# Performance work log

Hardware: AMD Instinct MI355X
Metric: run time of the kernel (lower is better)

## Reference

```python
import jax, jax.numpy as jnp
import numpy as np

N_AE = 64
N_GRAPHS = 4096
N_ELE = 16384
EPS = 1e-5


def _seg_mean(v, idx, num_segments):
    s = jax.ops.segment_sum(v, idx, num_segments=num_segments)
    c = jax.ops.segment_sum(jnp.ones((v.shape[0], 1), v.dtype), idx, num_segments=num_segments)
    return s / jnp.maximum(c, 1.0)


def _batchnorm(h, gamma, beta):
    mu = jnp.mean(h, axis=0)
    var = jnp.mean(jnp.square(h - mu), axis=0)  # biased, as torch BN training fwd
    return (h - mu) * jax.lax.rsqrt(var + EPS) * gamma + beta


def _dist_layer(x, dist_feat, atom_idx, ele_idx, W, b, gamma, beta):
    # x: [N, 2*n_ae]
    pa = jax.nn.relu(_seg_mean(x[:, :N_AE], atom_idx, N_GRAPHS))[atom_idx]   # [N, n_ae]
    pe = jax.nn.relu(_seg_mean(x[:, N_AE:], ele_idx, N_ELE))[ele_idx]        # [N, n_ae]
    h = jnp.concatenate([dist_feat, pa, pe], axis=1)                          # [N, n_de+2*n_ae]
    h = h @ W.T + b                                                           # [N, 2*n_ae]
    h = _batchnorm(h, gamma, beta)
    return jax.nn.relu(h + x)


def setup_inputs() -> dict:
    key = jax.random.key(0)
    ks = jax.random.split(key, 12)
    N = 500000
    n_re = 64
    n_be = 64
    d = 2 * N_AE
    inp = {
        "x": jax.random.normal(ks[0], (N, d), jnp.float32),
        "rdf_feat": jax.random.normal(ks[1], (N, n_re), jnp.float32),
        "bdf_feat": jax.random.normal(ks[2], (N, n_be), jnp.float32),
        "atom_idx": jnp.sort(jax.random.randint(ks[3], (N,), 0, N_GRAPHS)),
        "ele_idx": jax.random.randint(ks[4], (N,), 0, N_ELE),
        "rdf_W": jax.random.normal(ks[5], (d, n_re + d), jnp.float32) * 0.05,
        "rdf_b": jnp.zeros((d,), jnp.float32),
        "rdf_gamma": jnp.ones((d,), jnp.float32),
        "rdf_beta": jnp.zeros((d,), jnp.float32),
        "bdf_W": jax.random.normal(ks[6], (d, n_be + d), jnp.float32) * 0.05,
        "bdf_b": jnp.zeros((d,), jnp.float32),
        "bdf_gamma": jnp.ones((d,), jnp.float32),
        "bdf_beta": jnp.zeros((d,), jnp.float32),
        "fc_W": jax.random.normal(ks[7], (d, 2 * d), jnp.float32) * 0.05,
        "fc_b": jnp.zeros((d,), jnp.float32),
    }
    return inp


def reference(x, rdf_feat, bdf_feat, atom_idx, ele_idx,
              rdf_W, rdf_b, rdf_gamma, rdf_beta,
              bdf_W, bdf_b, bdf_gamma, bdf_beta,
              fc_W, fc_b):
    x1 = _dist_layer(x, rdf_feat, atom_idx, ele_idx, rdf_W, rdf_b, rdf_gamma, rdf_beta)
    x2 = _dist_layer(x, bdf_feat, atom_idx, ele_idx, bdf_W, bdf_b, bdf_gamma, bdf_beta)
    h = jnp.concatenate([x1, x2], axis=1)  # [N, 4*n_ae]
    return jax.nn.relu(h @ fc_W.T + fc_b)  # [N, 2*n_ae]
```

## Files before the change

### kernel.cpp

```cpp
#include <hip/hip_runtime.h>
#include <hip/hip_bf16.h>

#define N_GRAPHS 4096
#define N_ELE 16384
#define EPS 1e-5f

#define A_TAB_OFF 0
#define A_CNT_OFF 262144
#define E_TAB_OFF 266240
#define E_CNT_OFF 1314816
#define STAT_OFF  1331200
#define ZERO_WORDS 1347584
#define A_TABH_OFF 1347584
#define E_TABH_OFF 1478656
#define W1PK_OFF  2002944
#define FCPK_OFF  2027520
#define SCALE_OFF 2043904
#define SHIFT_OFF 2044160
#define WS_WORDS  2044416

typedef __attribute__((ext_vector_type(8))) short bf16x8;
typedef __attribute__((ext_vector_type(4))) float f32x4;

__device__ __forceinline__ float bf2f(unsigned s) { return __uint_as_float(s << 16); }
__device__ __forceinline__ unsigned f2bf(float f) {
  unsigned u = __float_as_uint(f);
  return (u + 0x7fffu + ((u >> 16) & 1u)) >> 16;
}

__global__ void k_prep(const float* __restrict__ W1, const float* __restrict__ W2,
                       const float* __restrict__ fcW, float* __restrict__ ws) {
  int tid = blockIdx.x * 512 + threadIdx.x;
  if (tid < 49152) {
    unsigned short* wpk = (unsigned short*)(ws + W1PK_OFF);
    int L = tid / 24576, rem = tid % 24576;
    int ct = rem / 3072, rem2 = rem % 3072;
    int i = rem2 >> 9, lane = (rem2 >> 3) & 63, j = rem2 & 7;
    int zkb = L ? (i + 2) : (i < 2 ? i : i + 2);
    int zk = zkb * 32 + ((lane >> 4) << 3) + j;
    int kp = L ? (zk - 64) : (zk < 64 ? zk : zk - 64);
    int col = ct * 16 + (lane & 15);
    const float* W = L ? W2 : W1;
    wpk[tid] = (unsigned short)f2bf(W[col * 192 + kp]);
  } else {
    int idx = tid - 49152;
    unsigned short* fpk = (unsigned short*)(ws + FCPK_OFF);
    int ct = idx >> 12, kb = (idx >> 9) & 7, lane = (idx >> 3) & 63, j = idx & 7;
    fpk[idx] = (unsigned short)f2bf(fcW[(ct * 16 + (lane & 15)) * 256 + kb * 32 + ((lane >> 4) << 3) + j]);
  }
}

__global__ void k_seg(const float* __restrict__ x, const int* __restrict__ aidx,
                      const int* __restrict__ eidx, float* __restrict__ ws, int N) {
  float* A_tab = ws + A_TAB_OFF; float* A_cnt = ws + A_CNT_OFF;
  float* E_tab = ws + E_TAB_OFF; float* E_cnt = ws + E_CNT_OFF;
  int t = threadIdx.x;
  int c = t & 63, p = (t >> 6) & 1, s = t >> 7;
  int r0 = blockIdx.x * 256;
  int rend = min(r0 + 256, N);
  if (p == 0) {
    float acc = 0.f, cnt = 0.f; int cur = -1;
    for (int r = r0 + s; r < rend; r += 2) {
      int a = aidx[r];
      float v = x[(size_t)r * 128 + c];
      if (a != cur) {
        if (cur >= 0) { atomicAdd(&A_tab[cur * 64 + c], acc); if (c == 0) atomicAdd(&A_cnt[cur], cnt); }
        cur = a; acc = v; cnt = 1.f;
      } else { acc += v; cnt += 1.f; }
    }
    if (cur >= 0) { atomicAdd(&A_tab[cur * 64 + c], acc); if (c == 0) atomicAdd(&A_cnt[cur], cnt); }
  } else {
    for (int r = r0 + s; r < rend; r += 2) {
      int e = eidx[r];
      float v = x[(size_t)r * 128 + 64 + c];
      atomicAdd(&E_tab[e * 64 + c], v);
      if (c == 0) atomicAdd(&E_cnt[e], 1.f);
    }
  }
}

__global__ void k_fin(float* __restrict__ ws) {
  int i = blockIdx.x * 256 + threadIdx.x;
  unsigned* w32 = (unsigned*)ws;
  if (i < 131072) {
    int e = 2 * i;
    float cnt = fmaxf(ws[A_CNT_OFF + (e >> 6)], 1.f);
    float v0 = fmaxf(ws[A_TAB_OFF + e] / cnt, 0.f);
    float v1 = fmaxf(ws[A_TAB_OFF + e + 1] / cnt, 0.f);
    w32[A_TABH_OFF + i] = f2bf(v0) | (f2bf(v1) << 16);
  }
  if (i < 524288) {
    int e = 2 * i;
    float cnt = fmaxf(ws[E_CNT_OFF + (e >> 6)], 1.f);
    float v0 = fmaxf(ws[E_TAB_OFF + e] / cnt, 0.f);
    float v1 = fmaxf(ws[E_TAB_OFF + e + 1] / cnt, 0.f);
    w32[E_TABH_OFF + i] = f2bf(v0) | (f2bf(v1) << 16);
  }
}

__global__ __launch_bounds__(512) void k_gemm(
    const float* __restrict__ rdf, const float* __restrict__ bdf,
    const int* __restrict__ aidx, const int* __restrict__ eidx,
    float* __restrict__ ws, unsigned* __restrict__ outp, int N) {
  __shared__ __align__(16) char smem[33792];
  const unsigned short* Atabh = (const unsigned short*)(ws + A_TABH_OFF);
  const unsigned short* Etabh = (const unsigned short*)(ws + E_TABH_OFF);
  int t = threadIdx.x;
  int row0 = blockIdx.x * 64;
  {
    int r = t >> 3, g = t & 7;
    int row = row0 + r;
    unsigned wv[16];
    if (row < N) {
      if (g < 4) {
        const float* src = ((g < 2) ? rdf : bdf) + (size_t)row * 64 + (g & 1) * 32;
        #pragma unroll
        for (int i = 0; i < 8; ++i) {
          float4 f = ((const float4*)src)[i];
          wv[i * 2]     = f2bf(f.x) | (f2bf(f.y) << 16);
          wv[i * 2 + 1] = f2bf(f.z) | (f2bf(f.w) << 16);
        }
      } else {
        const unsigned short* tab = (g < 6) ? Atabh : Etabh;
        int idx = (g < 6) ? aidx[row] : eidx[row];
        const uint4* srcv = (const uint4*)(tab + (size_t)idx * 64 + (g & 1) * 32);
        #pragma unroll
        for (int i = 0; i < 4; ++i) ((uint4*)wv)[i] = srcv[i];
      }
    } else {
      #pragma unroll
      for (int i = 0; i < 16; ++i) wv[i] = 0u;
    }
    int zc0 = g * 32;
    #pragma unroll
    for (int i = 0; i < 4; ++i) {
      int byte = r * 512 + (((zc0 + i * 8) * 2) ^ ((r & 7) << 4));
      *(uint4*)(smem + byte) = ((uint4*)wv)[i];
    }
  }
  __syncthreads();
  int l = t & 63, w = t >> 6;
  int L = w >> 2, ctp = w & 3;
  f32x4 acc[4][2];
  #pragma unroll
  for (int mt = 0; mt < 4; ++mt)
    #pragma unroll
    for (int cti = 0; cti < 2; ++cti) acc[mt][cti] = (f32x4){0.f, 0.f, 0.f, 0.f};
  const unsigned short* Wpk = (const unsigned short*)(ws + W1PK_OFF) + L * 24576;
  #pragma unroll
  for (int i = 0; i < 6; ++i) {
    int zkb = L ? (i + 2) : (i < 2 ? i : i + 2);
    bf16x8 af[4];
    #pragma unroll
    for (int mt = 0; mt < 4; ++mt) {
      int rr = mt * 16 + (l & 15);
      int byte = rr * 512 + ((zkb * 64 + ((l >> 4) << 4)) ^ ((rr & 7) << 4));
      af[mt] = *(const bf16x8*)(smem + byte);
    }
    #pragma unroll
    for (int cti = 0; cti < 2; ++cti) {
      int ct = ctp * 2 + cti;
      bf16x8 bfr = *(const bf16x8*)(Wpk + ((ct * 6 + i) * 64 + l) * 8);
      #pragma unroll
      for (int mt = 0; mt < 4; ++mt)
        acc[mt][cti] = __builtin_amdgcn_mfma_f32_16x16x32_bf16(af[mt], bfr, acc[mt][cti], 0, 0, 0);
    }
  }
  float ssum[2], ssq[2];
  #pragma unroll
  for (int cti = 0; cti < 2; ++cti) {
    float s = 0.f, q = 0.f;
    #pragma unroll
    for (int mt = 0; mt < 4; ++mt)
      #pragma unroll
      for (int rr = 0; rr < 4; ++rr) { float v = acc[mt][cti][rr]; s += v; q += v * v; }
    s += __shfl_xor(s, 16); s += __shfl_xor(s, 32);
    q += __shfl_xor(q, 16); q += __shfl_xor(q, 32);
    ssum[cti] = s; ssq[cti] = q;
  }
  {
    float* stat = ws + STAT_OFF + (blockIdx.x & 31) * 512;
    if (l < 16) {
      #pragma unroll
      for (int cti = 0; cti < 2; ++cti) {
        int gc = L * 128 + ctp * 32 + cti * 16 + l;
        atomicAdd(&stat[gc], ssum[cti]);
        atomicAdd(&stat[256 + gc], ssq[cti]);
      }
    }
  }
  __syncthreads();
  unsigned* hl = (unsigned*)smem;
  #pragma unroll
  for (int mt = 0; mt < 4; ++mt)
    #pragma unroll
    for (int cti = 0; cti < 2; ++cti)
      #pragma unroll
      for (int rr = 0; rr < 4; ++rr) {
        unsigned ub = f2bf(acc[mt][cti][rr]);
        unsigned pb = (unsigned)__shfl_xor((int)ub, 1);
        if (!(l & 1)) {
          int orow = mt * 16 + ((l >> 4) << 2) + rr;
          int colp = (L * 128 + ctp * 32 + cti * 16 + (l & 15)) >> 1;
          hl[orow * 132 + colp] = ub | (pb << 16);
        }
      }
  __syncthreads();
  #pragma unroll
  for (int p = 0; p < 4; ++p) {
    int e = p * 512 + t;
    int rr = e >> 5, v4 = e & 31;
    if (row0 + rr < N)
      ((uint4*)outp)[(size_t)(row0 + rr) * 32 + v4] = *(uint4*)&hl[rr * 132 + v4 * 4];
  }
}

__global__ void k_bnfin(const float* __restrict__ g1, const float* __restrict__ b1,
                        const float* __restrict__ g2, const float* __restrict__ b2,
                        float* __restrict__ ws, int N) {
  int c = threadIdx.x;
  float s = 0.f, q = 0.f;
  for (int m = 0; m < 32; ++m) { s += ws[STAT_OFF + m * 512 + c]; q += ws[STAT_OFF + m * 512 + 256 + c]; }
  float inv = 1.f / (float)N;
  float mu = s * inv;
  float var = fmaxf(q * inv - mu * mu, 0.f);
  int lyr = c >> 7, cc = c & 127;
  float ga = lyr ? g2[cc] : g1[cc];
  float be = lyr ? b2[cc] : b1[cc];
  float sc = ga * rsqrtf(var + EPS);
  ws[SCALE_OFF + c] = sc;
  ws[SHIFT_OFF + c] = be - mu * sc;
}

__global__ __launch_bounds__(512) void k_fc(
    const float* __restrict__ x, const float* __restrict__ fcb,
    float* __restrict__ ws, float* __restrict__ out, int N) {
  __shared__ __align__(16) char smem[33792];
  __shared__ float scsh[512];
  int t = threadIdx.x;
  int row0 = blockIdx.x * 64;
  scsh[t] = ws[SCALE_OFF + t];
  const unsigned* hp = (const unsigned*)out;
  int r = t >> 3, g = t & 7;
  int row = row0 + r;
  unsigned hw[16]; float xr[32];
  if (row < N) {
    #pragma unroll
    for (int i = 0; i < 4; ++i) ((uint4*)hw)[i] = ((const uint4*)(hp + (size_t)row * 128 + g * 16))[i];
    #pragma unroll
    for (int i = 0; i < 8; ++i) ((float4*)xr)[i] = ((const float4*)(x + (size_t)row * 128 + (g & 3) * 32))[i];
  } else {
    #pragma unroll
    for (int i = 0; i < 16; ++i) hw[i] = 0u;
    #pragma unroll
    for (int i = 0; i < 32; ++i) xr[i] = 0.f;
  }
  __syncthreads();
  {
    unsigned outw[16];
    if (row < N) {
      #pragma unroll
      for (int j = 0; j < 16; ++j) {
        int c = g * 32 + 2 * j;
        float lo = bf2f(hw[j] & 0xffffu) * scsh[c] + scsh[256 + c] + xr[2 * j];
        float hi = bf2f(hw[j] >> 16) * scsh[c + 1] + scsh[256 + c + 1] + xr[2 * j + 1];
        outw[j] = f2bf(fmaxf(lo, 0.f)) | (f2bf(fmaxf(hi, 0.f)) << 16);
      }
    } else {
      #pragma unroll
      for (int j = 0; j < 16; ++j) outw[j] = 0u;
    }
    #pragma unroll
    for (int i = 0; i < 4; ++i) {
      int byte = r * 512 + (((g * 32 + i * 8) * 2) ^ ((r & 7) << 4));
      *(uint4*)(smem + byte) = ((uint4*)outw)[i];
    }
  }
  __syncthreads();
  int l = t & 63, w = t >> 6;
  f32x4 acc[4];
  #pragma unroll
  for (int mt = 0; mt < 4; ++mt) acc[mt] = (f32x4){0.f, 0.f, 0.f, 0.f};
  const unsigned short* Fpk = (const unsigned short*)(ws + FCPK_OFF);
  #pragma unroll
  for (int kb = 0; kb < 8; ++kb) {
    bf16x8 bfr = *(const bf16x8*)(Fpk + ((w * 8 + kb) * 64 + l) * 8);
    #pragma unroll
    for (int mt = 0; mt < 4; ++mt) {
      int rr = mt * 16 + (l & 15);
      int byte = rr * 512 + ((kb * 64 + ((l >> 4) << 4)) ^ ((rr & 7) << 4));
      bf16x8 af = *(const bf16x8*)(smem + byte);
      acc[mt] = __builtin_amdgcn_mfma_f32_16x16x32_bf16(af, bfr, acc[mt], 0, 0, 0);
    }
  }
  float bias = fcb[(w << 4) + (l & 15)];
  __syncthreads();
  float* ol = (float*)smem;
  #pragma unroll
  for (int mt = 0; mt < 4; ++mt)
    #pragma unroll
    for (int rr = 0; rr < 4; ++rr)
      ol[(mt * 16 + ((l >> 4) << 2) + rr) * 132 + (w << 4) + (l & 15)] = fmaxf(acc[mt][rr] + bias, 0.f);
  __syncthreads();
  #pragma unroll
  for (int p = 0; p < 4; ++p) {
    int e = p * 512 + t;
    int rr = e >> 5, v4 = e & 31;
    if (row0 + rr < N)
      ((float4*)out)[(size_t)(row0 + rr) * 32 + v4] = *(float4*)&ol[rr * 132 + v4 * 4];
  }
}

extern "C" void kernel_launch(void* const* d_in, const int* in_sizes, int n_in,
                              void* d_out, int out_size, void* d_ws, size_t ws_size,
                              hipStream_t stream) {
  const float* x    = (const float*)d_in[0];
  const float* rdf  = (const float*)d_in[1];
  const float* bdf  = (const float*)d_in[2];
  const int*   aidx = (const int*)d_in[3];
  const int*   eidx = (const int*)d_in[4];
  const float* rdfW = (const float*)d_in[5];
  const float* rdfG = (const float*)d_in[7];
  const float* rdfBe= (const float*)d_in[8];
  const float* bdfW = (const float*)d_in[9];
  const float* bdfG = (const float*)d_in[11];
  const float* bdfBe= (const float*)d_in[12];
  const float* fcW  = (const float*)d_in[13];
  const float* fcB  = (const float*)d_in[14];
  float* out = (float*)d_out;
  float* ws  = (float*)d_ws;
  int N = in_sizes[0] / 128;

  hipMemsetAsync(d_ws, 0, (size_t)ZERO_WORDS * 4, stream);
  k_prep<<<160, 512, 0, stream>>>(rdfW, bdfW, fcW, ws);
  k_seg<<<(N + 255) / 256, 256, 0, stream>>>(x, aidx, eidx, ws, N);
  k_fin<<<2048, 256, 0, stream>>>(ws);
  int tiles = (N + 63) / 64;
  k_gemm<<<tiles, 512, 0, stream>>>(rdf, bdf, aidx, eidx, ws, (unsigned*)d_out, N);
  k_bnfin<<<1, 256, 0, stream>>>(rdfG, rdfBe, bdfG, bdfBe, ws, N);
  k_fc<<<tiles, 512, 0, stream>>>(x, fcB, ws, out, N);
}
```

Baseline: 472.2 us.

## Make GEMM and FC kernels persistent with double-buffered register prefetch

Both k_gemm and k_fc now launch a fixed grid of 512 persistent blocks that loop over 64-row tiles. While MFMA work runs on the current tile, the next tile's global loads, and the indices two tiles ahead, are prefetched into registers, then converted into a second 32KB LDS buffer. The LDS swizzle changes to an XOR slot scheme without padding, and bf16 conversion moves to the HIP intrinsic. The aim is to hide global load latency behind compute and avoid per-block launch cost. The cost is 64KB of LDS and more register pressure, which may limit occupancy; launch_bounds now asks for 4 waves.

```diff
diff --git a/kernel.cpp b/kernel.cpp
--- a/kernel.cpp
+++ b/kernel.cpp
@@ -27,6 +27,12 @@
   unsigned u = __float_as_uint(f);
   return (u + 0x7fffu + ((u >> 16) & 1u)) >> 16;
 }
+__device__ __forceinline__ unsigned pkbf(float a, float b) {
+  union { __hip_bfloat16 h; unsigned short u; } ca, cb;
+  ca.h = __float2bfloat16(a); cb.h = __float2bfloat16(b);
+  return (unsigned)ca.u | ((unsigned)cb.u << 16);
+}
+
 
 __global__ void k_prep(const float* __restrict__ W1, const float* __restrict__ W2,
                        const float* __restrict__ fcW, float* __restrict__ ws) {
@@ -98,120 +104,158 @@
   }
 }
 
-__global__ __launch_bounds__(512) void k_gemm(
+__device__ __forceinline__ void load_tile(const float* __restrict__ rdf, const float* __restrict__ bdf,
+    const unsigned short* __restrict__ Atabh, const unsigned short* __restrict__ Etabh,
+    int row, bool ok, int g, int idx, float4* fv) {
+  if (g < 4) {
+    if (ok) {
+      const float4* src = (const float4*)(((g < 2) ? rdf : bdf) + (size_t)row * 64 + (g & 1) * 32);
+      #pragma unroll
+      for (int i = 0; i < 8; ++i) fv[i] = src[i];
+    } else {
+      #pragma unroll
+      for (int i = 0; i < 8; ++i) fv[i] = (float4){0.f, 0.f, 0.f, 0.f};
+    }
+  } else {
+    if (ok) {
+      const float4* src = (const float4*)(((g < 6) ? Atabh : Etabh) + (size_t)idx * 64 + (g & 1) * 32);
+      #pragma unroll
+      for (int i = 0; i < 4; ++i) fv[i] = src[i];
+    } else {
+      #pragma unroll
+      for (int i = 0; i < 4; ++i) fv[i] = (float4){0.f, 0.f, 0.f, 0.f};
+    }
+  }
+}
+
+__device__ __forceinline__ void cvt_write(char* buf, int r, int g, const float4* fv) {
+  unsigned wv[16];
+  if (g < 4) {
+    #pragma unroll
+    for (int i = 0; i < 8; ++i) {
+      wv[2 * i]     = pkbf(fv[i].x, fv[i].y);
+      wv[2 * i + 1] = pkbf(fv[i].z, fv[i].w);
+    }
+  } else {
+    #pragma unroll
+    for (int i = 0; i < 4; ++i) ((float4*)wv)[i] = fv[i];
+  }
+  #pragma unroll
+  for (int i = 0; i < 4; ++i) {
+    int slot = ((g ^ r ^ i) & 7) | (i << 3);
+    *(uint4*)(buf + r * 512 + slot * 16) = ((uint4*)wv)[i];
+  }
+}
+
+__global__ __launch_bounds__(512, 4) void k_gemm(
     const float* __restrict__ rdf, const float* __restrict__ bdf,
     const int* __restrict__ aidx, const int* __restrict__ eidx,
-    float* __restrict__ ws, unsigned* __restrict__ outp, int N) {
-  __shared__ __align__(16) char smem[33792];
+    float* __restrict__ ws, unsigned* __restrict__ outp, int N, int nT) {
+  __shared__ __align__(16) char smem[65536];
   const unsigned short* Atabh = (const unsigned short*)(ws + A_TABH_OFF);
   const unsigned short* Etabh = (const unsigned short*)(ws + E_TABH_OFF);
   int t = threadIdx.x;
-  int row0 = blockIdx.x * 64;
+  int l = t & 63, w = t >> 6;
+  int r = t >> 3, g = t & 7;
+  int L = w >> 2, ctp = w & 3;
+  const unsigned short* WpkL = (const unsigned short*)(ws + W1PK_OFF) + L * 24576;
+  float* stat = ws + STAT_OFF + (blockIdx.x & 31) * 512;
+  int step = gridDim.x;
+  int tile = blockIdx.x;
+  float4 fv[8];
   {
-    int r = t >> 3, g = t & 7;
-    int row = row0 + r;
-    unsigned wv[16];
-    if (row < N) {
-      if (g < 4) {
-        const float* src = ((g < 2) ? rdf : bdf) + (size_t)row * 64 + (g & 1) * 32;
+    int row = tile * 64 + r; bool ok = row < N;
+    int idx0 = 0;
+    if (g >= 4 && ok) idx0 = ((g < 6) ? aidx : eidx)[row];
+    load_tile(rdf, bdf, Atabh, Etabh, row, ok, g, idx0, fv);
+  }
+  int idxN = 0;
+  {
+    int t2 = tile + step; int row2 = t2 * 64 + r;
+    if (g >= 4 && t2 < nT && row2 < N) idxN = ((g < 6) ? aidx : eidx)[row2];
+  }
+  cvt_write(smem, r, g, fv);
+  __syncthreads();
+  int cur = 0;
+  while (true) {
+    int nxt = tile + step;
+    bool hasN = nxt < nT;
+    int idxN2 = 0;
+    if (hasN) {
+      int row = nxt * 64 + r; bool ok = row < N;
+      load_tile(rdf, bdf, Atabh, Etabh, row, ok, g, idxN, fv);
+      int t3 = nxt + step; int row3 = t3 * 64 + r;
+      if (g >= 4 && t3 < nT && row3 < N) idxN2 = ((g < 6) ? aidx : eidx)[row3];
+    }
+    char* buf = smem + cur * 32768;
+    f32x4 acc[4][2];
+    #pragma unroll
+    for (int mt = 0; mt < 4; ++mt)
+      #pragma unroll
+      for (int cti = 0; cti < 2; ++cti) acc[mt][cti] = (f32x4){0.f, 0.f, 0.f, 0.f};
+    #pragma unroll
+    for (int i = 0; i < 6; ++i) {
+      int zkb = L ? (i + 2) : (i < 2 ? i : i + 2);
+      bf16x8 af[4];
+      #pragma unroll
+      for (int mt = 0; mt < 4; ++mt) {
+        int rr = mt * 16 + (l & 15);
+        int slot = ((zkb ^ rr ^ (l >> 4)) & 7) | ((l >> 4) << 3);
+        af[mt] = *(const bf16x8*)(buf + rr * 512 + slot * 16);
+      }
+      #pragma unroll
+      for (int cti = 0; cti < 2; ++cti) {
+        bf16x8 bfr = *(const bf16x8*)(WpkL + (((ctp * 2 + cti) * 6 + i) * 64 + l) * 8);
         #pragma unroll
-        for (int i = 0; i < 8; ++i) {
-          float4 f = ((const float4*)src)[i];
-          wv[i * 2]     = f2bf(f.x) | (f2bf(f.y) << 16);
-          wv[i * 2 + 1] = f2bf(f.z) | (f2bf(f.w) << 16);
+        for (int mt = 0; mt < 4; ++mt)
+          acc[mt][cti] = __builtin_amdgcn_mfma_f32_16x16x32_bf16(af[mt], bfr, acc[mt][cti], 0, 0, 0);
+      }
+    }
+    #pragma unroll
+    for (int cti = 0; cti < 2; ++cti) {
+      float s = 0.f, q = 0.f;
+      #pragma unroll
+      for (int mt = 0; mt < 4; ++mt)
+        #pragma unroll
+        for (int rr = 0; rr < 4; ++rr) { float v = acc[mt][cti][rr]; s += v; q += v * v; }
+      s += __shfl_xor(s, 16); s += __shfl_xor(s, 32);
+      q += __shfl_xor(q, 16); q += __shfl_xor(q, 32);
+      if (l < 16) {
+        int gc = L * 128 + ctp * 32 + cti * 16 + l;
+        atomicAdd(&stat[gc], s);
+        atomicAdd(&stat[256 + gc], q);
+      }
+    }
+    __syncthreads();
+    #pragma unroll
+    for (int mt = 0; mt < 4; ++mt)
+      #pragma unroll
+      for (int cti = 0; cti < 2; ++cti)
+        #pragma unroll
+        for (int rr = 0; rr < 4; ++rr) {
+          unsigned ub = pkbf(acc[mt][cti][rr], 0.f) & 0xffffu;
+          unsigned pb = (unsigned)__shfl_xor((int)ub, 1);
+          if (!(l & 1)) {
+            int orow = mt * 16 + ((l >> 4) << 2) + rr;
+            int colp = (L * 128 + ctp * 32 + cti * 16 + (l & 15)) >> 1;
+            int c = colp >> 2;
+            int ec = ((c ^ orow) & 7) | (c & 24);
+            *(unsigned*)(buf + orow * 512 + ec * 16 + (colp & 3) * 4) = ub | (pb << 16);
+          }
         }
-      } else {
-        const unsigned short* tab = (g < 6) ? Atabh : Etabh;
-        int idx = (g < 6) ? aidx[row] : eidx[row];
-        const uint4* srcv = (const uint4*)(tab + (size_t)idx * 64 + (g & 1) * 32);
-        #pragma unroll
-        for (int i = 0; i < 4; ++i) ((uint4*)wv)[i] = srcv[i];
-      }
-    } else {
-      #pragma unroll
-      for (int i = 0; i < 16; ++i) wv[i] = 0u;
-    }
-    int zc0 = g * 32;
-    #pragma unroll
-    for (int i = 0; i < 4; ++i) {
-      int byte = r * 512 + (((zc0 + i * 8) * 2) ^ ((r & 7) << 4));
-      *(uint4*)(smem + byte) = ((uint4*)wv)[i];
-    }
-  }
-  __syncthreads();
-  int l = t & 63, w = t >> 6;
-  int L = w >> 2, ctp = w & 3;
-  f32x4 acc[4][2];
-  #pragma unroll
-  for (int mt = 0; mt < 4; ++mt)
-    #pragma unroll
-    for (int cti = 0; cti < 2; ++cti) acc[mt][cti] = (f32x4){0.f, 0.f, 0.f, 0.f};
-  const unsigned short* Wpk = (const unsigned short*)(ws + W1PK_OFF) + L * 24576;
-  #pragma unroll
-  for (int i = 0; i < 6; ++i) {
-    int zkb = L ? (i + 2) : (i < 2 ? i : i + 2);
-    bf16x8 af[4];
-    #pragma unroll
-    for (int mt = 0; mt < 4; ++mt) {
-      int rr = mt * 16 + (l & 15);
-      int byte = rr * 512 + ((zkb * 64 + ((l >> 4) << 4)) ^ ((rr & 7) << 4));
-      af[mt] = *(const bf16x8*)(smem + byte);
-    }
-    #pragma unroll
-    for (int cti = 0; cti < 2; ++cti) {
-      int ct = ctp * 2 + cti;
-      bf16x8 bfr = *(const bf16x8*)(Wpk + ((ct * 6 + i) * 64 + l) * 8);
-      #pragma unroll
-      for (int mt = 0; mt < 4; ++mt)
-        acc[mt][cti] = __builtin_amdgcn_mfma_f32_16x16x32_bf16(af[mt], bfr, acc[mt][cti], 0, 0, 0);
-    }
-  }
-  float ssum[2], ssq[2];
-  #pragma unroll
-  for (int cti = 0; cti < 2; ++cti) {
-    float s = 0.f, q = 0.f;
-    #pragma unroll
-    for (int mt = 0; mt < 4; ++mt)
-      #pragma unroll
-      for (int rr = 0; rr < 4; ++rr) { float v = acc[mt][cti][rr]; s += v; q += v * v; }
-    s += __shfl_xor(s, 16); s += __shfl_xor(s, 32);
-    q += __shfl_xor(q, 16); q += __shfl_xor(q, 32);
-    ssum[cti] = s; ssq[cti] = q;
-  }
-  {
-    float* stat = ws + STAT_OFF + (blockIdx.x & 31) * 512;
-    if (l < 16) {
-      #pragma unroll
-      for (int cti = 0; cti < 2; ++cti) {
-        int gc = L * 128 + ctp * 32 + cti * 16 + l;
-        atomicAdd(&stat[gc], ssum[cti]);
-        atomicAdd(&stat[256 + gc], ssq[cti]);
-      }
-    }
-  }
-  __syncthreads();
-  unsigned* hl = (unsigned*)smem;
-  #pragma unroll
-  for (int mt = 0; mt < 4; ++mt)
-    #pragma unroll
-    for (int cti = 0; cti < 2; ++cti)
-      #pragma unroll
-      for (int rr = 0; rr < 4; ++rr) {
-        unsigned ub = f2bf(acc[mt][cti][rr]);
-        unsigned pb = (unsigned)__shfl_xor((int)ub, 1);
-        if (!(l & 1)) {
-          int orow = mt * 16 + ((l >> 4) << 2) + rr;
-          int colp = (L * 128 + ctp * 32 + cti * 16 + (l & 15)) >> 1;
-          hl[orow * 132 + colp] = ub | (pb << 16);
-        }
-      }
-  __syncthreads();
-  #pragma unroll
-  for (int p = 0; p < 4; ++p) {
-    int e = p * 512 + t;
-    int rr = e >> 5, v4 = e & 31;
-    if (row0 + rr < N)
-      ((uint4*)outp)[(size_t)(row0 + rr) * 32 + v4] = *(uint4*)&hl[rr * 132 + v4 * 4];
+    __syncthreads();
+    int row0 = tile * 64;
+    #pragma unroll
+    for (int p = 0; p < 4; ++p) {
+      int e = p * 512 + t; int rr = e >> 5, v4 = e & 31;
+      int ec = ((v4 ^ rr) & 7) | (v4 & 24);
+      uint4 val = *(const uint4*)(buf + rr * 512 + ec * 16);
+      if (row0 + rr < N) ((uint4*)outp)[(size_t)(row0 + rr) * 32 + v4] = val;
+    }
+    if (!hasN) break;
+    cvt_write(smem + (cur ^ 1) * 32768, r, g, fv);
+    __syncthreads();
+    tile = nxt; cur ^= 1; idxN = idxN2;
   }
 }
 
@@ -232,82 +276,108 @@
   ws[SHIFT_OFF + c] = be - mu * sc;
 }
 
-__global__ __launch_bounds__(512) void k_fc(
+__device__ __forceinline__ void load_fc(const unsigned* __restrict__ hp, const float* __restrict__ x,
+    int row, bool ok, int g, uint4* hv, float4* xv) {
+  if (ok) {
+    const uint4* hs = (const uint4*)(hp + (size_t)row * 128 + g * 16);
+    #pragma unroll
+    for (int i = 0; i < 4; ++i) hv[i] = hs[i];
+    const float4* xs = (const float4*)(x + (size_t)row * 128 + (g & 3) * 32);
+    #pragma unroll
+    for (int i = 0; i < 8; ++i) xv[i] = xs[i];
+  } else {
+    #pragma unroll
+    for (int i = 0; i < 4; ++i) hv[i] = (uint4){0u, 0u, 0u, 0u};
+    #pragma unroll
+    for (int i = 0; i < 8; ++i) xv[i] = (float4){0.f, 0.f, 0.f, 0.f};
+  }
+}
+
+__device__ __forceinline__ void proc_write(char* buf, int r, int g,
+    const uint4* hv, const float4* xv, const float* scsh) {
+  unsigned wv[16];
+  const unsigned* hu = (const unsigned*)hv;
+  const float* xf = (const float*)xv;
+  #pragma unroll
+  for (int j = 0; j < 16; ++j) {
+    int c = g * 32 + 2 * j;
+    float lo = bf2f(hu[j] & 0xffffu) * scsh[c]     + scsh[256 + c]     + xf[2 * j];
+    float hi = bf2f(hu[j] >> 16)     * scsh[c + 1] + scsh[256 + c + 1] + xf[2 * j + 1];
+    wv[j] = pkbf(fmaxf(lo, 0.f), fmaxf(hi, 0.f));
+  }
+  #pragma unroll
+  for (int i = 0; i < 4; ++i) {
+    int slot = ((g ^ r ^ i) & 7) | (i << 3);
+    *(uint4*)(buf + r * 512 + slot * 16) = ((uint4*)wv)[i];
+  }
+}
+
+__global__ __launch_bounds__(512, 4) void k_fc(
     const float* __restrict__ x, const float* __restrict__ fcb,
-    float* __restrict__ ws, float* __restrict__ out, int N) {
-  __shared__ __align__(16) char smem[33792];
+    float* __restrict__ ws, float* __restrict__ out, int N, int nT) {
+  __shared__ __align__(16) char smem[65536];
   __shared__ float scsh[512];
   int t = threadIdx.x;
-  int row0 = blockIdx.x * 64;
+  int l = t & 63, w = t >> 6;
+  int r = t >> 3, g = t & 7;
   scsh[t] = ws[SCALE_OFF + t];
+  const unsigned short* Fpk = (const unsigned short*)(ws + FCPK_OFF);
   const unsigned* hp = (const unsigned*)out;
-  int r = t >> 3, g = t & 7;
-  int row = row0 + r;
-  unsigned hw[16]; float xr[32];
-  if (row < N) {
-    #pragma unroll
-    for (int i = 0; i < 4; ++i) ((uint4*)hw)[i] = ((const uint4*)(hp + (size_t)row * 128 + g * 16))[i];
-    #pragma unroll
-    for (int i = 0; i < 8; ++i) ((float4*)xr)[i] = ((const float4*)(x + (size_t)row * 128 + (g & 3) * 32))[i];
-  } else {
-    #pragma unroll
-    for (int i = 0; i < 16; ++i) hw[i] = 0u;
-    #pragma unroll
-    for (int i = 0; i < 32; ++i) xr[i] = 0.f;
-  }
-  __syncthreads();
-  {
-    unsigned outw[16];
-    if (row < N) {
-      #pragma unroll
-      for (int j = 0; j < 16; ++j) {
-        int c = g * 32 + 2 * j;
-        float lo = bf2f(hw[j] & 0xffffu) * scsh[c] + scsh[256 + c] + xr[2 * j];
-        float hi = bf2f(hw[j] >> 16) * scsh[c + 1] + scsh[256 + c + 1] + xr[2 * j + 1];
-        outw[j] = f2bf(fmaxf(lo, 0.f)) | (f2bf(fmaxf(hi, 0.f)) << 16);
-      }
-    } else {
-      #pragma unroll
-      for (int j = 0; j < 16; ++j) outw[j] = 0u;
-    }
-    #pragma unroll
-    for (int i = 0; i < 4; ++i) {
-      int byte = r * 512 + (((g * 32 + i * 8) * 2) ^ ((r & 7) << 4));
-      *(uint4*)(smem + byte) = ((uint4*)outw)[i];
-    }
-  }
-  __syncthreads();
-  int l = t & 63, w = t >> 6;
-  f32x4 acc[4];
-  #pragma unroll
-  for (int mt = 0; mt < 4; ++mt) acc[mt] = (f32x4){0.f, 0.f, 0.f, 0.f};
-  const unsigned short* Fpk = (const unsigned short*)(ws + FCPK_OFF);
-  #pragma unroll
-  for (int kb = 0; kb < 8; ++kb) {
-    bf16x8 bfr = *(const bf16x8*)(Fpk + ((w * 8 + kb) * 64 + l) * 8);
-    #pragma unroll
-    for (int mt = 0; mt < 4; ++mt) {
-      int rr = mt * 16 + (l & 15);
-      int byte = rr * 512 + ((kb * 64 + ((l >> 4) << 4)) ^ ((rr & 7) << 4));
-      bf16x8 af = *(const bf16x8*)(smem + byte);
-      acc[mt] = __builtin_amdgcn_mfma_f32_16x16x32_bf16(af, bfr, acc[mt], 0, 0, 0);
-    }
-  }
+  int step = gridDim.x;
+  int tile = blockIdx.x;
+  uint4 hv[4]; float4 xv[8];
+  load_fc(hp, x, tile * 64 + r, (tile * 64 + r) < N, g, hv, xv);
   float bias = fcb[(w << 4) + (l & 15)];
   __syncthreads();
-  float* ol = (float*)smem;
-  #pragma unroll
-  for (int mt = 0; mt < 4; ++mt)
-    #pragma unroll
-    for (int rr = 0; rr < 4; ++rr)
-      ol[(mt * 16 + ((l >> 4) << 2) + rr) * 132 + (w << 4) + (l & 15)] = fmaxf(acc[mt][rr] + bias, 0.f);
+  proc_write(smem, r, g, hv, xv, scsh);
   __syncthreads();
-  #pragma unroll
-  for (int p = 0; p < 4; ++p) {
-    int e = p * 512 + t;
-    int rr = e >> 5, v4 = e & 31;
-    if (row0 + rr < N)
-      ((float4*)out)[(size_t)(row0 + rr) * 32 + v4] = *(float4*)&ol[rr * 132 + v4 * 4];
+  int cur = 0;
+  while (true) {
+    int nxt = tile + step;
+    bool hasN = nxt < nT;
+    if (hasN) {
+      int row = nxt * 64 + r;
+      load_fc(hp, x, row, row < N, g, hv, xv);
+    }
+    char* buf = smem + cur * 32768;
+    f32x4 acc[4];
+    #pragma unroll
+    for (int mt = 0; mt < 4; ++mt) acc[mt] = (f32x4){0.f, 0.f, 0.f, 0.f};
+    #pragma unroll
+    for (int kb = 0; kb < 8; ++kb) {
+      bf16x8 bfr = *(const bf16x8*)(Fpk + ((w * 8 + kb) * 64 + l) * 8);
+      #pragma unroll
+      for (int mt = 0; mt < 4; ++mt) {
+        int rr = mt * 16 + (l & 15);
+        int slot = ((kb ^ rr ^ (l >> 4)) & 7) | ((l >> 4) << 3);
+        bf16x8 af = *(const bf16x8*)(buf + rr * 512 + slot * 16);
+        acc[mt] = __builtin_amdgcn_mfma_f32_16x16x32_bf16(af, bfr, acc[mt], 0, 0, 0);
+      }
+    }
+    __syncthreads();
+    #pragma unroll
+    for (int mt = 0; mt < 4; ++mt)
+      #pragma unroll
+      for (int rr = 0; rr < 4; ++rr) {
+        int orow = mt * 16 + ((l >> 4) << 2) + rr;
+        int col = (w << 4) + (l & 15);
+        int c = col >> 2;
+        int ec = ((c ^ orow) & 7) | (c & 24);
+        *(float*)(buf + orow * 512 + ec * 16 + (col & 3) * 4) = fmaxf(acc[mt][rr] + bias, 0.f);
+      }
+    __syncthreads();
+    int row0 = tile * 64;
+    #pragma unroll
+    for (int p = 0; p < 4; ++p) {
+      int e = p * 512 + t; int rr = e >> 5, v4 = e & 31;
+      int ec = ((v4 ^ rr) & 7) | (v4 & 24);
+      float4 val = *(const float4*)(buf + rr * 512 + ec * 16);
+      if (row0 + rr < N) ((float4*)out)[(size_t)(row0 + rr) * 32 + v4] = val;
+    }
+    if (!hasN) break;
+    proc_write(smem + (cur ^ 1) * 32768, r, g, hv, xv, scsh);
+    __syncthreads();
+    tile = nxt; cur ^= 1;
   }
 }
 
@@ -330,13 +400,14 @@
   float* out = (float*)d_out;
   float* ws  = (float*)d_ws;
   int N = in_sizes[0] / 128;
+  int nT = (N + 63) / 64;
+  int grid = 512; if (grid > nT) grid = nT;
 
   hipMemsetAsync(d_ws, 0, (size_t)ZERO_WORDS * 4, stream);
   k_prep<<<160, 512, 0, stream>>>(rdfW, bdfW, fcW, ws);
   k_seg<<<(N + 255) / 256, 256, 0, stream>>>(x, aidx, eidx, ws, N);
   k_fin<<<2048, 256, 0, stream>>>(ws);
-  int tiles = (N + 63) / 64;
-  k_gemm<<<tiles, 512, 0, stream>>>(rdf, bdf, aidx, eidx, ws, (unsigned*)d_out, N);
+  k_gemm<<<grid, 512, 0, stream>>>(rdf, bdf, aidx, eidx, ws, (unsigned*)d_out, N, nT);
   k_bnfin<<<1, 256, 0, stream>>>(rdfG, rdfBe, bdfG, bdfBe, ws, N);
-  k_fc<<<tiles, 512, 0, stream>>>(x, fcB, ws, out, N);
-}
+  k_fc<<<grid, 512, 0, stream>>>(x, fcB, ws, out, N, nT);
+}
```

New measurement: 888.8 us. +88.2%, slower.

## Gather segment-mean rows directly into LDS and reswizzle shared tiles

Applied to the files above, without the earlier changes.

The gemm kernel now gathers the per-atom and per-element bf16 table rows straight into LDS with global_load_lds, with a zeroed workspace pad serving out-of-range rows. The dense rdf/bdf features are split into separate 16-byte chunks with an XOR swizzle. Padded LDS staging is replaced by XOR-swizzled 512-byte rows in both kernels, which cuts shared memory per block and aims to avoid bank conflicts. Manual bf16 rounding is swapped for the library conversion, and k_fc loads are reordered so the global reads are issued before the scale load. The cost targeted is register round-trips and address math on the gather path, at the price of more complex indexing and reliance on the async LDS load builtin.

```diff
diff --git a/kernel.cpp b/kernel.cpp
--- a/kernel.cpp
+++ b/kernel.cpp
@@ -10,14 +10,15 @@
 #define E_TAB_OFF 266240
 #define E_CNT_OFF 1314816
 #define STAT_OFF  1331200
-#define ZERO_WORDS 1347584
-#define A_TABH_OFF 1347584
-#define E_TABH_OFF 1478656
-#define W1PK_OFF  2002944
-#define FCPK_OFF  2027520
-#define SCALE_OFF 2043904
-#define SHIFT_OFF 2044160
-#define WS_WORDS  2044416
+#define ZPAD_OFF  1347584
+#define ZERO_WORDS 1347588
+#define A_TABH_OFF 1347600
+#define E_TABH_OFF 1478672
+#define W1PK_OFF  2002960
+#define FCPK_OFF  2027536
+#define SCALE_OFF 2043920
+#define SHIFT_OFF 2044176
+#define WS_WORDS  2044432
 
 typedef __attribute__((ext_vector_type(8))) short bf16x8;
 typedef __attribute__((ext_vector_type(4))) float f32x4;
@@ -27,6 +28,17 @@
   unsigned u = __float_as_uint(f);
   return (u + 0x7fffu + ((u >> 16) & 1u)) >> 16;
 }
+__device__ __forceinline__ unsigned pkbf(float a, float b) {
+  union { __hip_bfloat16 h; unsigned short u; } ca, cb;
+  ca.h = __float2bfloat16(a); cb.h = __float2bfloat16(b);
+  return (unsigned)ca.u | ((unsigned)cb.u << 16);
+}
+__device__ __forceinline__ void gload16(const void* g, void* l) {
+  __builtin_amdgcn_global_load_lds(
+      (const __attribute__((address_space(1))) unsigned*)g,
+      (__attribute__((address_space(3))) unsigned*)l, 16, 0, 0);
+}
+
 
 __global__ void k_prep(const float* __restrict__ W1, const float* __restrict__ W2,
                        const float* __restrict__ fcW, float* __restrict__ ws) {
@@ -102,71 +114,86 @@
     const float* __restrict__ rdf, const float* __restrict__ bdf,
     const int* __restrict__ aidx, const int* __restrict__ eidx,
     float* __restrict__ ws, unsigned* __restrict__ outp, int N) {
-  __shared__ __align__(16) char smem[33792];
+  __shared__ __align__(16) char smem[32768];
   const unsigned short* Atabh = (const unsigned short*)(ws + A_TABH_OFF);
   const unsigned short* Etabh = (const unsigned short*)(ws + E_TABH_OFF);
+  const void* zpad = (const void*)(ws + ZPAD_OFF);
   int t = threadIdx.x;
+  int l = t & 63, w = t >> 6;
   int row0 = blockIdx.x * 64;
+
+  #pragma unroll
+  for (int ii = 0; ii < 2; ++ii) {
+    int rb = (w * 2 + ii) * 4;
+    int r = rb + (l >> 4);
+    int srow = row0 + r;
+    bool ok = srow < N;
+    int s = l & 15;
+    int c = (s & 8) | ((s ^ r) & 7);
+    const void* src;
+    if (c < 8) {
+      int ia = ok ? aidx[srow] : 0;
+      src = (const void*)(Atabh + ((size_t)ia * 64 + c * 8));
+    } else {
+      int ie = ok ? eidx[srow] : 0;
+      src = (const void*)(Etabh + ((size_t)ie * 64 + (c - 8) * 8));
+    }
+    if (!ok) src = zpad;
+    gload16(src, smem + 16384 + rb * 256);
+  }
+
   {
-    int r = t >> 3, g = t & 7;
+    int r = t >> 3, c0 = (t & 7) * 2;
     int row = row0 + r;
-    unsigned wv[16];
-    if (row < N) {
-      if (g < 4) {
-        const float* src = ((g < 2) ? rdf : bdf) + (size_t)row * 64 + (g & 1) * 32;
-        #pragma unroll
-        for (int i = 0; i < 8; ++i) {
-          float4 f = ((const float4*)src)[i];
-          wv[i * 2]     = f2bf(f.x) | (f2bf(f.y) << 16);
-          wv[i * 2 + 1] = f2bf(f.z) | (f2bf(f.w) << 16);
-        }
-      } else {
-        const unsigned short* tab = (g < 6) ? Atabh : Etabh;
-        int idx = (g < 6) ? aidx[row] : eidx[row];
-        const uint4* srcv = (const uint4*)(tab + (size_t)idx * 64 + (g & 1) * 32);
-        #pragma unroll
-        for (int i = 0; i < 4; ++i) ((uint4*)wv)[i] = srcv[i];
-      }
-    } else {
-      #pragma unroll
-      for (int i = 0; i < 16; ++i) wv[i] = 0u;
-    }
-    int zc0 = g * 32;
-    #pragma unroll
-    for (int i = 0; i < 4; ++i) {
-      int byte = r * 512 + (((zc0 + i * 8) * 2) ^ ((r & 7) << 4));
-      *(uint4*)(smem + byte) = ((uint4*)wv)[i];
-    }
-  }
-  __syncthreads();
-  int l = t & 63, w = t >> 6;
+    bool ok = row < N;
+    #pragma unroll
+    for (int cc = 0; cc < 2; ++cc) {
+      int c = c0 + cc;
+      uint4 wv;
+      if (ok) {
+        const float4* src = (const float4*)(c < 8 ? rdf + (size_t)row * 64 + c * 8
+                                                  : bdf + (size_t)row * 64 + (c - 8) * 8);
+        float4 f0 = src[0], f1 = src[1];
+        wv.x = pkbf(f0.x, f0.y); wv.y = pkbf(f0.z, f0.w);
+        wv.z = pkbf(f1.x, f1.y); wv.w = pkbf(f1.z, f1.w);
+      } else wv = (uint4){0u, 0u, 0u, 0u};
+      int slot = (c & 8) | ((c ^ r) & 7);
+      *(uint4*)(smem + r * 256 + slot * 16) = wv;
+    }
+  }
+  __syncthreads();
+
   int L = w >> 2, ctp = w & 3;
+  const unsigned short* WpkL = (const unsigned short*)(ws + W1PK_OFF) + L * 24576;
   f32x4 acc[4][2];
   #pragma unroll
   for (int mt = 0; mt < 4; ++mt)
     #pragma unroll
     for (int cti = 0; cti < 2; ++cti) acc[mt][cti] = (f32x4){0.f, 0.f, 0.f, 0.f};
-  const unsigned short* Wpk = (const unsigned short*)(ws + W1PK_OFF) + L * 24576;
+  int half = l >> 4;
   #pragma unroll
   for (int i = 0; i < 6; ++i) {
     int zkb = L ? (i + 2) : (i < 2 ? i : i + 2);
+    int cg = zkb * 4 + half;
+    const char* base = smem + (zkb < 4 ? 0 : 16384);
+    int cl = cg & 15;
     bf16x8 af[4];
     #pragma unroll
     for (int mt = 0; mt < 4; ++mt) {
       int rr = mt * 16 + (l & 15);
-      int byte = rr * 512 + ((zkb * 64 + ((l >> 4) << 4)) ^ ((rr & 7) << 4));
-      af[mt] = *(const bf16x8*)(smem + byte);
+      int slot = (cl & 8) | ((cl ^ rr) & 7);
+      af[mt] = *(const bf16x8*)(base + rr * 256 + slot * 16);
     }
     #pragma unroll
     for (int cti = 0; cti < 2; ++cti) {
-      int ct = ctp * 2 + cti;
-      bf16x8 bfr = *(const bf16x8*)(Wpk + ((ct * 6 + i) * 64 + l) * 8);
+      bf16x8 bfr = *(const bf16x8*)(WpkL + (((ctp * 2 + cti) * 6 + i) * 64 + l) * 8);
       #pragma unroll
       for (int mt = 0; mt < 4; ++mt)
         acc[mt][cti] = __builtin_amdgcn_mfma_f32_16x16x32_bf16(af[mt], bfr, acc[mt][cti], 0, 0, 0);
     }
   }
-  float ssum[2], ssq[2];
+
+  float* stat = ws + STAT_OFF + (blockIdx.x & 31) * 512;
   #pragma unroll
   for (int cti = 0; cti < 2; ++cti) {
     float s = 0.f, q = 0.f;
@@ -176,42 +203,37 @@
       for (int rr = 0; rr < 4; ++rr) { float v = acc[mt][cti][rr]; s += v; q += v * v; }
     s += __shfl_xor(s, 16); s += __shfl_xor(s, 32);
     q += __shfl_xor(q, 16); q += __shfl_xor(q, 32);
-    ssum[cti] = s; ssq[cti] = q;
-  }
-  {
-    float* stat = ws + STAT_OFF + (blockIdx.x & 31) * 512;
     if (l < 16) {
-      #pragma unroll
-      for (int cti = 0; cti < 2; ++cti) {
-        int gc = L * 128 + ctp * 32 + cti * 16 + l;
-        atomicAdd(&stat[gc], ssum[cti]);
-        atomicAdd(&stat[256 + gc], ssq[cti]);
-      }
-    }
-  }
-  __syncthreads();
-  unsigned* hl = (unsigned*)smem;
+      int gc = L * 128 + ctp * 32 + cti * 16 + l;
+      atomicAdd(&stat[gc], s);
+      atomicAdd(&stat[256 + gc], q);
+    }
+  }
+  __syncthreads();
+
   #pragma unroll
   for (int mt = 0; mt < 4; ++mt)
     #pragma unroll
     for (int cti = 0; cti < 2; ++cti)
       #pragma unroll
       for (int rr = 0; rr < 4; ++rr) {
-        unsigned ub = f2bf(acc[mt][cti][rr]);
+        unsigned ub = pkbf(acc[mt][cti][rr], 0.f) & 0xffffu;
         unsigned pb = (unsigned)__shfl_xor((int)ub, 1);
         if (!(l & 1)) {
           int orow = mt * 16 + ((l >> 4) << 2) + rr;
           int colp = (L * 128 + ctp * 32 + cti * 16 + (l & 15)) >> 1;
-          hl[orow * 132 + colp] = ub | (pb << 16);
+          int c = colp >> 2;
+          int ec = ((c ^ orow) & 7) | (c & 24);
+          *(unsigned*)(smem + orow * 512 + ec * 16 + (colp & 3) * 4) = ub | (pb << 16);
         }
       }
   __syncthreads();
   #pragma unroll
   for (int p = 0; p < 4; ++p) {
-    int e = p * 512 + t;
-    int rr = e >> 5, v4 = e & 31;
-    if (row0 + rr < N)
-      ((uint4*)outp)[(size_t)(row0 + rr) * 32 + v4] = *(uint4*)&hl[rr * 132 + v4 * 4];
+    int e = p * 512 + t; int rr = e >> 5, v4 = e & 31;
+    int ec = ((v4 ^ rr) & 7) | (v4 & 24);
+    uint4 val = *(const uint4*)(smem + rr * 512 + ec * 16);
+    if (row0 + rr < N) ((uint4*)outp)[(size_t)(row0 + rr) * 32 + v4] = val;
   }
 }
 
@@ -235,79 +257,84 @@
 __global__ __launch_bounds__(512) void k_fc(
     const float* __restrict__ x, const float* __restrict__ fcb,
     float* __restrict__ ws, float* __restrict__ out, int N) {
-  __shared__ __align__(16) char smem[33792];
+  __shared__ __align__(16) char smem[32768];
   __shared__ float scsh[512];
   int t = threadIdx.x;
+  int l = t & 63, w = t >> 6;
+  int r = t >> 3, g = t & 7;
+  const unsigned* hp = (const unsigned*)out;
   int row0 = blockIdx.x * 64;
+  int row = row0 + r;
+  bool ok = row < N;
+  uint4 hv[4]; float4 xv[8];
+  if (ok) {
+    const uint4* hs = (const uint4*)(hp + (size_t)row * 128 + g * 16);
+    #pragma unroll
+    for (int i = 0; i < 4; ++i) hv[i] = hs[i];
+    const float4* xs = (const float4*)(x + (size_t)row * 128 + (g & 3) * 32);
+    #pragma unroll
+    for (int i = 0; i < 8; ++i) xv[i] = xs[i];
+  } else {
+    #pragma unroll
+    for (int i = 0; i < 4; ++i) hv[i] = (uint4){0u, 0u, 0u, 0u};
+    #pragma unroll
+    for (int i = 0; i < 8; ++i) xv[i] = (float4){0.f, 0.f, 0.f, 0.f};
+  }
   scsh[t] = ws[SCALE_OFF + t];
-  const unsigned* hp = (const unsigned*)out;
-  int r = t >> 3, g = t & 7;
-  int row = row0 + r;
-  unsigned hw[16]; float xr[32];
-  if (row < N) {
-    #pragma unroll
-    for (int i = 0; i < 4; ++i) ((uint4*)hw)[i] = ((const uint4*)(hp + (size_t)row * 128 + g * 16))[i];
-    #pragma unroll
-    for (int i = 0; i < 8; ++i) ((float4*)xr)[i] = ((const float4*)(x + (size_t)row * 128 + (g & 3) * 32))[i];
-  } else {
-    #pragma unroll
-    for (int i = 0; i < 16; ++i) hw[i] = 0u;
-    #pragma unroll
-    for (int i = 0; i < 32; ++i) xr[i] = 0.f;
-  }
   __syncthreads();
   {
-    unsigned outw[16];
-    if (row < N) {
-      #pragma unroll
-      for (int j = 0; j < 16; ++j) {
-        int c = g * 32 + 2 * j;
-        float lo = bf2f(hw[j] & 0xffffu) * scsh[c] + scsh[256 + c] + xr[2 * j];
-        float hi = bf2f(hw[j] >> 16) * scsh[c + 1] + scsh[256 + c + 1] + xr[2 * j + 1];
-        outw[j] = f2bf(fmaxf(lo, 0.f)) | (f2bf(fmaxf(hi, 0.f)) << 16);
-      }
-    } else {
-      #pragma unroll
-      for (int j = 0; j < 16; ++j) outw[j] = 0u;
+    unsigned wv[16];
+    const unsigned* hu = (const unsigned*)hv;
+    const float* xf = (const float*)xv;
+    #pragma unroll
+    for (int j = 0; j < 16; ++j) {
+      int c = g * 32 + 2 * j;
+      float lo = bf2f(hu[j] & 0xffffu) * scsh[c]     + scsh[256 + c]     + xf[2 * j];
+      float hi = bf2f(hu[j] >> 16)     * scsh[c + 1] + scsh[256 + c + 1] + xf[2 * j + 1];
+      wv[j] = pkbf(fmaxf(lo, 0.f), fmaxf(hi, 0.f));
     }
     #pragma unroll
     for (int i = 0; i < 4; ++i) {
-      int byte = r * 512 + (((g * 32 + i * 8) * 2) ^ ((r & 7) << 4));
-      *(uint4*)(smem + byte) = ((uint4*)outw)[i];
-    }
-  }
-  __syncthreads();
-  int l = t & 63, w = t >> 6;
+      int slot = ((g ^ r ^ i) & 7) | (i << 3);
+      *(uint4*)(smem + r * 512 + slot * 16) = ((uint4*)wv)[i];
+    }
+  }
+  __syncthreads();
   f32x4 acc[4];
   #pragma unroll
   for (int mt = 0; mt < 4; ++mt) acc[mt] = (f32x4){0.f, 0.f, 0.f, 0.f};
   const unsigned short* Fpk = (const unsigned short*)(ws + FCPK_OFF);
+  int half = l >> 4;
   #pragma unroll
   for (int kb = 0; kb < 8; ++kb) {
     bf16x8 bfr = *(const bf16x8*)(Fpk + ((w * 8 + kb) * 64 + l) * 8);
     #pragma unroll
     for (int mt = 0; mt < 4; ++mt) {
       int rr = mt * 16 + (l & 15);
-      int byte = rr * 512 + ((kb * 64 + ((l >> 4) << 4)) ^ ((rr & 7) << 4));
-      bf16x8 af = *(const bf16x8*)(smem + byte);
+      int slot = ((kb ^ rr ^ half) & 7) | (half << 3);
+      bf16x8 af = *(const bf16x8*)(smem + rr * 512 + slot * 16);
       acc[mt] = __builtin_amdgcn_mfma_f32_16x16x32_bf16(af, bfr, acc[mt], 0, 0, 0);
     }
   }
   float bias = fcb[(w << 4) + (l & 15)];
   __syncthreads();
-  float* ol = (float*)smem;
   #pragma unroll
   for (int mt = 0; mt < 4; ++mt)
     #pragma unroll
-    for (int rr = 0; rr < 4; ++rr)
-      ol[(mt * 16 + ((l >> 4) << 2) + rr) * 132 + (w << 4) + (l & 15)] = fmaxf(acc[mt][rr] + bias, 0.f);
+    for (int rr = 0; rr < 4; ++rr) {
+      int orow = mt * 16 + ((l >> 4) << 2) + rr;
+      int col = (w << 4) + (l & 15);
+      int c = col >> 2;
+      int ec = ((c ^ orow) & 7) | (c & 24);
+      *(float*)(smem + orow * 512 + ec * 16 + (col & 3) * 4) = fmaxf(acc[mt][rr] + bias, 0.f);
+    }
   __syncthreads();
   #pragma unroll
   for (int p = 0; p < 4; ++p) {
-    int e = p * 512 + t;
-    int rr = e >> 5, v4 = e & 31;
-    if (row0 + rr < N)
-      ((float4*)out)[(size_t)(row0 + rr) * 32 + v4] = *(float4*)&ol[rr * 132 + v4 * 4];
+    int e = p * 512 + t; int rr = e >> 5, v4 = e & 31;
+    int ec = ((v4 ^ rr) & 7) | (v4 & 24);
+    float4 val = *(const float4*)(smem + rr * 512 + ec * 16);
+    if (row0 + rr < N) ((float4*)out)[(size_t)(row0 + rr) * 32 + v4] = val;
   }
 }
 
@@ -330,13 +357,13 @@
   float* out = (float*)d_out;
   float* ws  = (float*)d_ws;
   int N = in_sizes[0] / 128;
+  int nT = (N + 63) / 64;
 
   hipMemsetAsync(d_ws, 0, (size_t)ZERO_WORDS * 4, stream);
   k_prep<<<160, 512, 0, stream>>>(rdfW, bdfW, fcW, ws);
   k_seg<<<(N + 255) / 256, 256, 0, stream>>>(x, aidx, eidx, ws, N);
   k_fin<<<2048, 256, 0, stream>>>(ws);
-  int tiles = (N + 63) / 64;
-  k_gemm<<<tiles, 512, 0, stream>>>(rdf, bdf, aidx, eidx, ws, (unsigned*)d_out, N);
+  k_gemm<<<nT, 512, 0, stream>>>(rdf, bdf, aidx, eidx, ws, (unsigned*)d_out, N);
   k_bnfin<<<1, 256, 0, stream>>>(rdfG, rdfBe, bdfG, bdfBe, ws, N);
-  k_fc<<<tiles, 512, 0, stream>>>(x, fcB, ws, out, N);
-}
+  k_fc<<<nT, 512, 0, stream>>>(x, fcB, ws, out, N);
+}
```

New measurement: 482.9 us. +2.3%, slower.
